# Optimization experiments

Measured on AMD Instinct MI355X. Metric: run time of the kernel, lower is better.

Reference implementation:

```python
import jax, jax.numpy as jnp
import numpy as np

B = 8192
LATENT = 512
HIDDEN = 256
MLP_HIDDEN = 1024
NUM_CLASSES = 2
ODE_STEPS = 100


def setup_inputs() -> dict:
    key = jax.random.key(0)
    ks = jax.random.split(key, 14)
    s = lambda fan_in: 1.0 / np.sqrt(fan_in)
    d = {
        "z": jax.random.normal(ks[0], (B, LATENT), dtype=jnp.float32),
        # real NeuralODE: Linear(latent+1 -> hidden) -> GELU -> Linear(hidden -> latent)
        "real_W1": jax.random.uniform(ks[1], (LATENT + 1, HIDDEN), jnp.float32, -s(LATENT + 1), s(LATENT + 1)),
        "real_b1": jax.random.uniform(ks[2], (HIDDEN,), jnp.float32, -s(LATENT + 1), s(LATENT + 1)),
        "real_W2": jax.random.uniform(ks[3], (HIDDEN, LATENT), jnp.float32, -s(HIDDEN), s(HIDDEN)),
        "real_b2": jax.random.uniform(ks[4], (LATENT,), jnp.float32, -s(HIDDEN), s(HIDDEN)),
        # fake NeuralODE
        "fake_W1": jax.random.uniform(ks[5], (LATENT + 1, HIDDEN), jnp.float32, -s(LATENT + 1), s(LATENT + 1)),
        "fake_b1": jax.random.uniform(ks[6], (HIDDEN,), jnp.float32, -s(LATENT + 1), s(LATENT + 1)),
        "fake_W2": jax.random.uniform(ks[7], (HIDDEN, LATENT), jnp.float32, -s(HIDDEN), s(HIDDEN)),
        "fake_b2": jax.random.uniform(ks[8], (LATENT,), jnp.float32, -s(HIDDEN), s(HIDDEN)),
        # classifier MLP: Linear(2*latent -> mlp_hidden) -> GELU -> Linear(mlp_hidden -> num_classes)
        "mlp_W1": jax.random.uniform(ks[9], (2 * LATENT, MLP_HIDDEN), jnp.float32, -s(2 * LATENT), s(2 * LATENT)),
        "mlp_b1": jax.random.uniform(ks[10], (MLP_HIDDEN,), jnp.float32, -s(2 * LATENT), s(2 * LATENT)),
        "mlp_W2": jax.random.uniform(ks[11], (MLP_HIDDEN, NUM_CLASSES), jnp.float32, -s(MLP_HIDDEN), s(MLP_HIDDEN)),
        "mlp_b2": jax.random.uniform(ks[12], (NUM_CLASSES,), jnp.float32, -s(MLP_HIDDEN), s(MLP_HIDDEN)),
    }
    return d


def _ode_net(z, t, W1, b1, W2, b2):
    # z: [B, latent], t: [B, 1] -> velocity [B, latent]
    inp = jnp.concatenate([z, t], axis=1)
    h = jax.nn.gelu(inp @ W1 + b1, approximate=False)
    return h @ W2 + b2


def _inv_sample(z, W1, b1, W2, b2, N):
    dt = 1.0 / N
    ones = jnp.ones((z.shape[0], 1), dtype=z.dtype)

    def step(z, i):
        t = ones * (i.astype(z.dtype) / N)  # [B, 1]
        pred = _ode_net(z, 1.0 - t, W1, b1, W2, b2)
        return z - pred * dt, None

    z, _ = jax.lax.scan(step, z, jnp.arange(N))
    return z


def reference(z, real_W1, real_b1, real_W2, real_b2,
              fake_W1, fake_b1, fake_W2, fake_b2,
              mlp_W1, mlp_b1, mlp_W2, mlp_b2):
    real_proj = _inv_sample(z, real_W1, real_b1, real_W2, real_b2, ODE_STEPS)
    fake_proj = _inv_sample(z, fake_W1, fake_b1, fake_W2, fake_b2, ODE_STEPS)
    combined = jnp.concatenate([real_proj, fake_proj], axis=1)  # [B, 2*latent]
    h = jax.nn.gelu(combined @ mlp_W1 + mlp_b1, approximate=False)
    logits = h @ mlp_W2 + mlp_b2  # [B, num_classes]
    return logits
```

## Files before the change

kernel.cpp:

```cpp
#include <hip/hip_runtime.h>
#include <hip/hip_bf16.h>

typedef __attribute__((ext_vector_type(8))) short short8;
typedef __attribute__((ext_vector_type(4))) short short4_;
typedef __attribute__((ext_vector_type(4))) float f32x4;
typedef __attribute__((ext_vector_type(2))) unsigned int uint2_;

#define MFMA16(a,b,c) __builtin_amdgcn_mfma_f32_16x16x32_bf16((a),(b),(c),0,0,0)

#define BAR() do {                                         \
  __builtin_amdgcn_sched_barrier(0);                       \
  asm volatile("s_waitcnt lgkmcnt(0)" ::: "memory");       \
  __builtin_amdgcn_s_barrier();                            \
  __builtin_amdgcn_sched_barrier(0);                       \
} while (0)

__device__ __forceinline__ short f2bf(float f){
  union { float f; unsigned u; } v; v.f = f;
  unsigned u = v.u;
  u = u + 0x7fffu + ((u >> 16) & 1u);
  return (short)(u >> 16);
}

__device__ __forceinline__ unsigned cvt_pk_bf16(float lo, float hi){
  unsigned r;
  asm("v_cvt_pk_bf16_f32 %0, %1, %2" : "=v"(r) : "v"(lo), "v"(hi));
  return r;
}

__device__ __forceinline__ float gelu_f(float x){
  float x2 = x * x;
  float t  = __builtin_fmaf(0.044715f, x2, 1.0f);
  float u  = 2.30211416f * x * t;
  float e  = __builtin_exp2f(u);
  float r  = __builtin_amdgcn_rcpf(e + 1.0f);
  return x * (1.0f - r);
}

__global__ void prep_kernel(
    const float* __restrict__ rW1, const float* __restrict__ rW2,
    const float* __restrict__ fW1, const float* __restrict__ fW2,
    const float* __restrict__ mW1,
    short* __restrict__ w1t_all, short* __restrict__ w2t_all,
    short* __restrict__ mw1t)
{
  int id = blockIdx.x * 256 + threadIdx.x;
  short8 v;
  if (id < 32768) {
    int l = id & 63, ks = (id >> 6) & 15, nt = (id >> 10) & 15, net = id >> 14;
    const float* W = net ? fW1 : rW1;
    int n  = nt * 16 + (l & 15);
    int k0 = ks * 32 + (l >> 4) * 8;
    #pragma unroll
    for (int j = 0; j < 8; ++j) v[j] = f2bf(W[(size_t)(k0 + j) * 256 + n]);
    *(short8*)(w1t_all + (size_t)id * 8) = v;
  } else if (id < 65536) {
    int id2 = id - 32768;
    int l = id2 & 63, ks = (id2 >> 6) & 7, nt = (id2 >> 9) & 31, net = id2 >> 14;
    const float* W = net ? fW2 : rW2;
    int n  = nt * 16 + (l & 15);
    int k0 = ks * 32 + (l >> 4) * 8;
    #pragma unroll
    for (int j = 0; j < 8; ++j) v[j] = f2bf(W[(size_t)(k0 + j) * 512 + n]);
    *(short8*)(w2t_all + (size_t)id2 * 8) = v;
  } else {
    int id3 = id - 65536;
    int l = id3 & 63, ks = (id3 >> 6) & 31, nt = id3 >> 11;
    int n  = nt * 16 + (l & 15);
    int k0 = ks * 32 + (l >> 4) * 8;
    #pragma unroll
    for (int j = 0; j < 8; ++j) v[j] = f2bf(mW1[(size_t)(k0 + j) * 1024 + n]);
    *(short8*)(mw1t + (size_t)id3 * 8) = v;
  }
}

#define LDW1(nt, ks) (*(const short8*)(w1t + ((size_t)(((2 * w + (nt)) * 16 + (ks)) * 64 + l) * 8)))
#define LDW2(nt, ks) (*(const short8*)(w2t + ((size_t)(((4 * w + (nt)) * 8  + (ks)) * 64 + l) * 8)))

__global__ __launch_bounds__(512) __attribute__((amdgpu_waves_per_eu(2)))
void ode_kernel(
    const float* __restrict__ z0,
    const short* __restrict__ w1t_all,
    const short* __restrict__ w2t_all,
    const float* __restrict__ rW1, const float* __restrict__ rb1, const float* __restrict__ rb2,
    const float* __restrict__ fW1, const float* __restrict__ fb1, const float* __restrict__ fb2,
    short* __restrict__ proj_all)
{
  __shared__ __align__(16) short zs[32768];
  __shared__ __align__(16) short hs[16384];
  __shared__ __align__(16) float cst[1024];

  const int blk = blockIdx.x;
  const int net = blk & 1;
  const int m0  = (blk >> 1) * 64;
  const int tid = threadIdx.x;
  const int w   = tid >> 6;
  const int l   = tid & 63;
  const int l4  = l & 15;
  const int g   = l >> 4;

  const short* w1t = w1t_all + net * 131072;
  const short* w2t = w2t_all + net * 131072;
  const float* b1p = net ? fb1 : rb1;
  const float* b2p = net ? fb2 : rb2;
  const float* w1r = (net ? fW1 : rW1) + 512 * 256;
  short* proj = proj_all + (size_t)net * (8192 * 512);

  if (tid < 256)       cst[tid] = b1p[tid];
  else                 cst[tid] = w1r[tid - 256];
  cst[512 + tid] = -0.01f * b2p[tid];

  f32x4 zacc[4][4];
  #pragma unroll
  for (int nt = 0; nt < 4; ++nt)
    #pragma unroll
    for (int mt = 0; mt < 4; ++mt)
      zacc[nt][mt] = *(const f32x4*)(z0 + (size_t)(m0 + 16 * mt + l4) * 512
                                        + (64 * w + 16 * nt + 4 * g));

  short8 pA0, pB0, pA1, pB1;
  short8 q00, q01, q02, q03;
  short8 q10, q11, q12, q13;

#define G1F(ks, pa, pb, ...) do {                                              \
    _Pragma("unroll")                                                          \
    for (int mt = 0; mt < 4; ++mt){                                            \
      int m  = 16 * mt + l4;                                                   \
      int kk = (ks) * 32 + 8 * g;                                              \
      short8 b = *(const short8*)((const char*)zs +                            \
                   (m * 1024 + ((kk * 2) ^ ((m & 7) << 4))));                  \
      hacc[0][mt] = MFMA16(pa, b, hacc[0][mt]);                                \
      hacc[1][mt] = MFMA16(pb, b, hacc[1][mt]);                                \
    }                                                                          \
    __VA_ARGS__;                                                               \
  } while (0)

#define G2K(ks, qa, qb, qc, qd, ...) do {                                      \
    _Pragma("unroll")                                                          \
    for (int mt = 0; mt < 4; ++mt){                                            \
      int m  = 16 * mt + l4;                                                   \
      int kk = (ks) * 32 + 8 * g;                                              \
      short8 b = *(const short8*)((const char*)hs +                            \
                   (m * 512 + ((kk * 2) ^ ((m & 7) << 4))));                   \
      zacc[0][mt] = MFMA16(qa, b, zacc[0][mt]);                                \
      zacc[1][mt] = MFMA16(qb, b, zacc[1][mt]);                                \
      zacc[2][mt] = MFMA16(qc, b, zacc[2][mt]);                                \
      zacc[3][mt] = MFMA16(qd, b, zacc[3][mt]);                                \
    }                                                                          \
    __VA_ARGS__;                                                               \
  } while (0)

#define GELU_STORE(NT) do {                                                    \
    f32x4 b1q = *(const f32x4*)&cst[32 * w + 16 * (NT) + 4 * g];               \
    f32x4 w1q = *(const f32x4*)&cst[256 + 32 * w + 16 * (NT) + 4 * g];         \
    _Pragma("unroll")                                                          \
    for (int mt = 0; mt < 4; ++mt){                                            \
      int m = 16 * mt + l4;                                                    \
      float gv[4];                                                             \
      _Pragma("unroll")                                                        \
      for (int r = 0; r < 4; ++r){                                             \
        float x  = hacc[NT][mt][r] + __builtin_fmaf(tw, w1q[r], b1q[r]);       \
        float x2 = x * x;                                                      \
        float tt = __builtin_fmaf(0.044715f, x2, 1.0f);                        \
        float uu = 2.30211416f * x * tt;                                       \
        float ee = __builtin_exp2f(uu);                                        \
        float rr = __builtin_amdgcn_rcpf(ee + 1.0f);                           \
        float xs = -0.01f * x;                                                 \
        gv[r] = __builtin_fmaf(-xs, rr, xs);                    \
      }                                                                        \
      uint2_ pk;                                                               \
      pk[0] = cvt_pk_bf16(gv[0], gv[1]);                                       \
      pk[1] = cvt_pk_bf16(gv[2], gv[3]);                                       \
      int nq = 32 * w + 16 * (NT) + 4 * g;                                     \
      int byte = m * 512 + ((nq * 2) ^ ((m & 7) << 4));                        \
      *(uint2_*)((char*)hs + byte) = pk;                                       \
    }                                                                          \
  } while (0)

  for (int i = 0; i < 100; ++i){
    float tw = 1.0f - 0.01f * (float)i;

    pA0 = LDW1(0, 0); pB0 = LDW1(1, 0);
    pA1 = LDW1(0, 1); pB1 = LDW1(1, 1);

    #pragma unroll
    for (int nt = 0; nt < 4; ++nt)
      #pragma unroll
      for (int mt = 0; mt < 4; ++mt){
        int m  = 16 * mt + l4;
        int kq = 64 * w + 16 * nt + 4 * g;
        uint2_ pk;
        pk[0] = cvt_pk_bf16(zacc[nt][mt][0], zacc[nt][mt][1]);
        pk[1] = cvt_pk_bf16(zacc[nt][mt][2], zacc[nt][mt][3]);
        int byte = m * 1024 + ((kq * 2) ^ ((m & 7) << 4));
        *(uint2_*)((char*)zs + byte) = pk;
      }
    BAR();

    f32x4 hacc[2][4];
    #pragma unroll
    for (int nt = 0; nt < 2; ++nt)
      #pragma unroll
      for (int mt = 0; mt < 4; ++mt) hacc[nt][mt] = (f32x4){0.f,0.f,0.f,0.f};

    G1F( 0, pA0, pB0, pA0 = LDW1(0, 2);  pB0 = LDW1(1, 2));
    G1F( 1, pA1, pB1, pA1 = LDW1(0, 3);  pB1 = LDW1(1, 3));
    G1F( 2, pA0, pB0, pA0 = LDW1(0, 4);  pB0 = LDW1(1, 4));
    G1F( 3, pA1, pB1, pA1 = LDW1(0, 5);  pB1 = LDW1(1, 5));
    G1F( 4, pA0, pB0, pA0 = LDW1(0, 6);  pB0 = LDW1(1, 6));
    G1F( 5, pA1, pB1, pA1 = LDW1(0, 7);  pB1 = LDW1(1, 7));
    G1F( 6, pA0, pB0, pA0 = LDW1(0, 8);  pB0 = LDW1(1, 8));
    G1F( 7, pA1, pB1, pA1 = LDW1(0, 9);  pB1 = LDW1(1, 9));
    G1F( 8, pA0, pB0, pA0 = LDW1(0,10);  pB0 = LDW1(1,10));
    G1F( 9, pA1, pB1, pA1 = LDW1(0,11);  pB1 = LDW1(1,11));
    G1F(10, pA0, pB0, pA0 = LDW1(0,12);  pB0 = LDW1(1,12));
    G1F(11, pA1, pB1, pA1 = LDW1(0,13);  pB1 = LDW1(1,13));
    G1F(12, pA0, pB0, pA0 = LDW1(0,14);  pB0 = LDW1(1,14));
    G1F(13, pA1, pB1, pA1 = LDW1(0,15);  pB1 = LDW1(1,15));
    G1F(14, pA0, pB0, );
    G1F(15, pA1, pB1, );

    q00 = LDW2(0,0); q01 = LDW2(1,0); q02 = LDW2(2,0); q03 = LDW2(3,0);

    GELU_STORE(0);
    GELU_STORE(1);

    q10 = LDW2(0,1); q11 = LDW2(1,1); q12 = LDW2(2,1); q13 = LDW2(3,1);
    BAR();

    G2K(0, q00, q01, q02, q03, q00=LDW2(0,2); q01=LDW2(1,2); q02=LDW2(2,2); q03=LDW2(3,2));
    G2K(1, q10, q11, q12, q13, q10=LDW2(0,3); q11=LDW2(1,3); q12=LDW2(2,3); q13=LDW2(3,3));
    G2K(2, q00, q01, q02, q03, q00=LDW2(0,4); q01=LDW2(1,4); q02=LDW2(2,4); q03=LDW2(3,4));
    G2K(3, q10, q11, q12, q13, q10=LDW2(0,5); q11=LDW2(1,5); q12=LDW2(2,5); q13=LDW2(3,5));
    G2K(4, q00, q01, q02, q03, q00=LDW2(0,6); q01=LDW2(1,6); q02=LDW2(2,6); q03=LDW2(3,6));
    G2K(5, q10, q11, q12, q13, q10=LDW2(0,7); q11=LDW2(1,7); q12=LDW2(2,7); q13=LDW2(3,7));
    G2K(6, q00, q01, q02, q03, );
    G2K(7, q10, q11, q12, q13, );

    #pragma unroll
    for (int nt = 0; nt < 4; ++nt){
      f32x4 b2q = *(const f32x4*)&cst[512 + 64 * w + 16 * nt + 4 * g];
      #pragma unroll
      for (int mt = 0; mt < 4; ++mt)
        #pragma unroll
        for (int r = 0; r < 4; ++r)
          zacc[nt][mt][r] += b2q[r];
    }
  }
#undef G1F
#undef G2K
#undef GELU_STORE

  #pragma unroll
  for (int nt = 0; nt < 4; ++nt)
    #pragma unroll
    for (int mt = 0; mt < 4; ++mt){
      int mg = m0 + 16 * mt + l4;
      int nq = 64 * w + 16 * nt + 4 * g;
      uint2_ pk;
      pk[0] = cvt_pk_bf16(zacc[nt][mt][0], zacc[nt][mt][1]);
      pk[1] = cvt_pk_bf16(zacc[nt][mt][2], zacc[nt][mt][3]);
      *(uint2_*)(proj + (size_t)mg * 512 + nq) = pk;
    }
}

__global__ __launch_bounds__(512, 2) void cls_kernel(
    const short* __restrict__ mw1t,
    const short* __restrict__ proj_all,
    const float* __restrict__ mb1,
    const float* __restrict__ mw2,
    const float* __restrict__ mb2,
    float* __restrict__ out)
{
  __shared__ __align__(16) float sb1[1024];
  __shared__ __align__(16) float sw2[2048];
  __shared__ __align__(16) float sred[2048];

  const int blk = blockIdx.x;
  const int m0  = blk * 32;
  const int tid = threadIdx.x;
  const int w = tid >> 6, l = tid & 63, l4 = l & 15, g = l >> 4;

  #pragma unroll
  for (int j = 0; j < 2; ++j) sb1[tid + 512 * j] = mb1[tid + 512 * j];
  #pragma unroll
  for (int j = 0; j < 4; ++j) sw2[tid + 512 * j] = mw2[tid + 512 * j];
  __syncthreads();

  float lacc[2][2] = {{0.f, 0.f}, {0.f, 0.f}};

  for (int rnd = 0; rnd < 4; ++rnd){
    f32x4 hacc[2][2];
    #pragma unroll
    for (int nt = 0; nt < 2; ++nt)
      #pragma unroll
      for (int mt = 0; mt < 2; ++mt)
        hacc[nt][mt] = (f32x4){0.f, 0.f, 0.f, 0.f};

    #pragma unroll
    for (int ks = 0; ks < 32; ++ks){
      int gnt0 = rnd * 16 + 2 * w;
      short8 a0 = *(const short8*)(mw1t + ((size_t)((gnt0    ) * 32 + ks) * 64 + l) * 8);
      short8 a1 = *(const short8*)(mw1t + ((size_t)((gnt0 + 1) * 32 + ks) * 64 + l) * 8);
      int k = ks * 32 + 8 * g;
      const short* src = (k < 512) ? (proj_all + k)
                                   : (proj_all + ((size_t)8192 * 512 - 512) + k);
      #pragma unroll
      for (int mt = 0; mt < 2; ++mt){
        int mg = m0 + 16 * mt + l4;
        short8 b = *(const short8*)(src + (size_t)mg * 512);
        hacc[0][mt] = MFMA16(a0, b, hacc[0][mt]);
        hacc[1][mt] = MFMA16(a1, b, hacc[1][mt]);
      }
    }
    #pragma unroll
    for (int nt = 0; nt < 2; ++nt){
      int nq = (rnd * 16 + 2 * w + nt) * 16 + 4 * g;
      f32x4 bb = *(const f32x4*)(sb1 + nq);
      #pragma unroll
      for (int r = 0; r < 4; ++r){
        float w2c0 = sw2[(nq + r) * 2 + 0];
        float w2c1 = sw2[(nq + r) * 2 + 1];
        #pragma unroll
        for (int mt = 0; mt < 2; ++mt){
          float x  = hacc[nt][mt][r] + bb[r];
          float gv = gelu_f(x);
          lacc[mt][0] = __builtin_fmaf(gv, w2c0, lacc[mt][0]);
          lacc[mt][1] = __builtin_fmaf(gv, w2c1, lacc[mt][1]);
        }
      }
    }
  }

  int part = w * 4 + g;
  #pragma unroll
  for (int mt = 0; mt < 2; ++mt)
    #pragma unroll
    for (int c = 0; c < 2; ++c)
      sred[((16 * mt + l4) * 2 + c) * 32 + part] = lacc[mt][c];
  __syncthreads();
  if (tid < 64){
    int m = tid >> 1, c = tid & 1;
    float s = 0.f;
    #pragma unroll
    for (int p2 = 0; p2 < 32; ++p2) s += sred[(m * 2 + c) * 32 + p2];
    out[(size_t)(m0 + m) * 2 + c] = s + mb2[c];
  }
}

extern "C" void kernel_launch(void* const* d_in, const int* in_sizes, int n_in,
                              void* d_out, int out_size, void* d_ws, size_t ws_size,
                              hipStream_t stream)
{
  const float* z0  = (const float*)d_in[0];
  const float* rW1 = (const float*)d_in[1];
  const float* rb1 = (const float*)d_in[2];
  const float* rW2 = (const float*)d_in[3];
  const float* rb2 = (const float*)d_in[4];
  const float* fW1 = (const float*)d_in[5];
  const float* fb1 = (const float*)d_in[6];
  const float* fW2 = (const float*)d_in[7];
  const float* fb2 = (const float*)d_in[8];
  const float* mW1 = (const float*)d_in[9];
  const float* mb1 = (const float*)d_in[10];
  const float* mW2 = (const float*)d_in[11];
  const float* mb2 = (const float*)d_in[12];
  float* out = (float*)d_out;

  char* ws = (char*)d_ws;
  short* w1t_all = (short*)(ws);
  short* w2t_all = (short*)(ws + 524288);
  short* mw1t    = (short*)(ws + 1048576);
  short* proj    = (short*)(ws + 3145728);

  prep_kernel<<<768, 256, 0, stream>>>(rW1, rW2, fW1, fW2, mW1, w1t_all, w2t_all, mw1t);
  ode_kernel<<<256, 512, 0, stream>>>(z0, w1t_all, w2t_all,
                                      rW1, rb1, rb2, fW1, fb1, fb2, proj);
  cls_kernel<<<256, 512, 0, stream>>>(mw1t, proj, mb1, mW2, mb2, out);
}
```

Before: 1.039 ms.

## Split ODE block rows across 16 waves instead of 8

Doubles the ODE kernel block to 1024 threads. Each wave now covers half of the 64-row tile (two m-tiles) for the same output columns, which halves per-wave accumulators and MFMA work per step. The goal is more waves per CU to hide LDS and weight-load latency across the 100 sequential steps. In exchange every wave reloads the same weight fragments from global/L2, so weight traffic per block doubles, and barriers now synchronise 16 waves.

```diff
diff --git a/kernel.cpp b/kernel.cpp
--- a/kernel.cpp
+++ b/kernel.cpp
@@ -74,11 +74,10 @@
   }
 }
 
-#define LDW1(nt, ks) (*(const short8*)(w1t + ((size_t)(((2 * w + (nt)) * 16 + (ks)) * 64 + l) * 8)))
-#define LDW2(nt, ks) (*(const short8*)(w2t + ((size_t)(((4 * w + (nt)) * 8  + (ks)) * 64 + l) * 8)))
-
-__global__ __launch_bounds__(512) __attribute__((amdgpu_waves_per_eu(2)))
-void ode_kernel(
+#define LDW1(nt, ks) (*(const short8*)(w1t + ((size_t)(((2 * wh + (nt)) * 16 + (ks)) * 64 + l) * 8)))
+#define LDW2(nt, ks) (*(const short8*)(w2t + ((size_t)(((4 * wh + (nt)) * 8  + (ks)) * 64 + l) * 8)))
+
+__global__ __launch_bounds__(1024) void ode_kernel(
     const float* __restrict__ z0,
     const short* __restrict__ w1t_all,
     const short* __restrict__ w2t_all,
@@ -95,6 +94,8 @@
   const int m0  = (blk >> 1) * 64;
   const int tid = threadIdx.x;
   const int w   = tid >> 6;
+  const int wh  = w & 7;
+  const int mh  = w >> 3;
   const int l   = tid & 63;
   const int l4  = l & 15;
   const int g   = l >> 4;
@@ -107,16 +108,16 @@
   short* proj = proj_all + (size_t)net * (8192 * 512);
 
   if (tid < 256)       cst[tid] = b1p[tid];
-  else                 cst[tid] = w1r[tid - 256];
-  cst[512 + tid] = -0.01f * b2p[tid];
-
-  f32x4 zacc[4][4];
+  else if (tid < 512)  cst[tid] = w1r[tid - 256];
+  else                 cst[tid] = -0.01f * b2p[tid - 512];
+
+  f32x4 zacc[4][2];
   #pragma unroll
   for (int nt = 0; nt < 4; ++nt)
     #pragma unroll
-    for (int mt = 0; mt < 4; ++mt)
-      zacc[nt][mt] = *(const f32x4*)(z0 + (size_t)(m0 + 16 * mt + l4) * 512
-                                        + (64 * w + 16 * nt + 4 * g));
+    for (int mtl = 0; mtl < 2; ++mtl)
+      zacc[nt][mtl] = *(const f32x4*)(z0 + (size_t)(m0 + 16 * (2 * mh + mtl) + l4) * 512
+                                         + (64 * wh + 16 * nt + 4 * g));
 
   short8 pA0, pB0, pA1, pB1;
   short8 q00, q01, q02, q03;
@@ -124,42 +125,42 @@
 
 #define G1F(ks, pa, pb, ...) do {                                              \
     _Pragma("unroll")                                                          \
-    for (int mt = 0; mt < 4; ++mt){                                            \
-      int m  = 16 * mt + l4;                                                   \
+    for (int mtl = 0; mtl < 2; ++mtl){                                         \
+      int m  = 16 * (2 * mh + mtl) + l4;                                       \
       int kk = (ks) * 32 + 8 * g;                                              \
       short8 b = *(const short8*)((const char*)zs +                            \
                    (m * 1024 + ((kk * 2) ^ ((m & 7) << 4))));                  \
-      hacc[0][mt] = MFMA16(pa, b, hacc[0][mt]);                                \
-      hacc[1][mt] = MFMA16(pb, b, hacc[1][mt]);                                \
+      hacc[0][mtl] = MFMA16(pa, b, hacc[0][mtl]);                              \
+      hacc[1][mtl] = MFMA16(pb, b, hacc[1][mtl]);                              \
     }                                                                          \
     __VA_ARGS__;                                                               \
   } while (0)
 
 #define G2K(ks, qa, qb, qc, qd, ...) do {                                      \
     _Pragma("unroll")                                                          \
-    for (int mt = 0; mt < 4; ++mt){                                            \
-      int m  = 16 * mt + l4;                                                   \
+    for (int mtl = 0; mtl < 2; ++mtl){                                         \
+      int m  = 16 * (2 * mh + mtl) + l4;                                       \
       int kk = (ks) * 32 + 8 * g;                                              \
       short8 b = *(const short8*)((const char*)hs +                            \
                    (m * 512 + ((kk * 2) ^ ((m & 7) << 4))));                   \
-      zacc[0][mt] = MFMA16(qa, b, zacc[0][mt]);                                \
-      zacc[1][mt] = MFMA16(qb, b, zacc[1][mt]);                                \
-      zacc[2][mt] = MFMA16(qc, b, zacc[2][mt]);                                \
-      zacc[3][mt] = MFMA16(qd, b, zacc[3][mt]);                                \
+      zacc[0][mtl] = MFMA16(qa, b, zacc[0][mtl]);                              \
+      zacc[1][mtl] = MFMA16(qb, b, zacc[1][mtl]);                              \
+      zacc[2][mtl] = MFMA16(qc, b, zacc[2][mtl]);                              \
+      zacc[3][mtl] = MFMA16(qd, b, zacc[3][mtl]);                              \
     }                                                                          \
     __VA_ARGS__;                                                               \
   } while (0)
 
 #define GELU_STORE(NT) do {                                                    \
-    f32x4 b1q = *(const f32x4*)&cst[32 * w + 16 * (NT) + 4 * g];               \
-    f32x4 w1q = *(const f32x4*)&cst[256 + 32 * w + 16 * (NT) + 4 * g];         \
+    f32x4 b1q = *(const f32x4*)&cst[32 * wh + 16 * (NT) + 4 * g];              \
+    f32x4 w1q = *(const f32x4*)&cst[256 + 32 * wh + 16 * (NT) + 4 * g];        \
     _Pragma("unroll")                                                          \
-    for (int mt = 0; mt < 4; ++mt){                                            \
-      int m = 16 * mt + l4;                                                    \
+    for (int mtl = 0; mtl < 2; ++mtl){                                         \
+      int m = 16 * (2 * mh + mtl) + l4;                                        \
       float gv[4];                                                             \
       _Pragma("unroll")                                                        \
       for (int r = 0; r < 4; ++r){                                             \
-        float x  = hacc[NT][mt][r] + __builtin_fmaf(tw, w1q[r], b1q[r]);       \
+        float x  = hacc[NT][mtl][r] + __builtin_fmaf(tw, w1q[r], b1q[r]);      \
         float x2 = x * x;                                                      \
         float tt = __builtin_fmaf(0.044715f, x2, 1.0f);                        \
         float uu = 2.30211416f * x * tt;                                       \
@@ -171,7 +172,7 @@
       uint2_ pk;                                                               \
       pk[0] = cvt_pk_bf16(gv[0], gv[1]);                                       \
       pk[1] = cvt_pk_bf16(gv[2], gv[3]);                                       \
-      int nq = 32 * w + 16 * (NT) + 4 * g;                                     \
+      int nq = 32 * wh + 16 * (NT) + 4 * g;                                    \
       int byte = m * 512 + ((nq * 2) ^ ((m & 7) << 4));                        \
       *(uint2_*)((char*)hs + byte) = pk;                                       \
     }                                                                          \
@@ -186,22 +187,22 @@
     #pragma unroll
     for (int nt = 0; nt < 4; ++nt)
       #pragma unroll
-      for (int mt = 0; mt < 4; ++mt){
-        int m  = 16 * mt + l4;
-        int kq = 64 * w + 16 * nt + 4 * g;
+      for (int mtl = 0; mtl < 2; ++mtl){
+        int m  = 16 * (2 * mh + mtl) + l4;
+        int kq = 64 * wh + 16 * nt + 4 * g;
         uint2_ pk;
-        pk[0] = cvt_pk_bf16(zacc[nt][mt][0], zacc[nt][mt][1]);
-        pk[1] = cvt_pk_bf16(zacc[nt][mt][2], zacc[nt][mt][3]);
+        pk[0] = cvt_pk_bf16(zacc[nt][mtl][0], zacc[nt][mtl][1]);
+        pk[1] = cvt_pk_bf16(zacc[nt][mtl][2], zacc[nt][mtl][3]);
         int byte = m * 1024 + ((kq * 2) ^ ((m & 7) << 4));
         *(uint2_*)((char*)zs + byte) = pk;
       }
     BAR();
 
-    f32x4 hacc[2][4];
+    f32x4 hacc[2][2];
     #pragma unroll
     for (int nt = 0; nt < 2; ++nt)
       #pragma unroll
-      for (int mt = 0; mt < 4; ++mt) hacc[nt][mt] = (f32x4){0.f,0.f,0.f,0.f};
+      for (int mtl = 0; mtl < 2; ++mtl) hacc[nt][mtl] = (f32x4){0.f,0.f,0.f,0.f};
 
     G1F( 0, pA0, pB0, pA0 = LDW1(0, 2);  pB0 = LDW1(1, 2));
     G1F( 1, pA1, pB1, pA1 = LDW1(0, 3);  pB1 = LDW1(1, 3));
@@ -239,12 +240,12 @@
 
     #pragma unroll
     for (int nt = 0; nt < 4; ++nt){
-      f32x4 b2q = *(const f32x4*)&cst[512 + 64 * w + 16 * nt + 4 * g];
-      #pragma unroll
-      for (int mt = 0; mt < 4; ++mt)
+      f32x4 b2q = *(const f32x4*)&cst[512 + 64 * wh + 16 * nt + 4 * g];
+      #pragma unroll
+      for (int mtl = 0; mtl < 2; ++mtl)
         #pragma unroll
         for (int r = 0; r < 4; ++r)
-          zacc[nt][mt][r] += b2q[r];
+          zacc[nt][mtl][r] += b2q[r];
     }
   }
 #undef G1F
@@ -254,12 +255,12 @@
   #pragma unroll
   for (int nt = 0; nt < 4; ++nt)
     #pragma unroll
-    for (int mt = 0; mt < 4; ++mt){
-      int mg = m0 + 16 * mt + l4;
-      int nq = 64 * w + 16 * nt + 4 * g;
+    for (int mtl = 0; mtl < 2; ++mtl){
+      int mg = m0 + 16 * (2 * mh + mtl) + l4;
+      int nq = 64 * wh + 16 * nt + 4 * g;
       uint2_ pk;
-      pk[0] = cvt_pk_bf16(zacc[nt][mt][0], zacc[nt][mt][1]);
-      pk[1] = cvt_pk_bf16(zacc[nt][mt][2], zacc[nt][mt][3]);
+      pk[0] = cvt_pk_bf16(zacc[nt][mtl][0], zacc[nt][mtl][1]);
+      pk[1] = cvt_pk_bf16(zacc[nt][mtl][2], zacc[nt][mtl][3]);
       *(uint2_*)(proj + (size_t)mg * 512 + nq) = pk;
     }
 }
@@ -374,7 +375,7 @@
   short* proj    = (short*)(ws + 3145728);
 
   prep_kernel<<<768, 256, 0, stream>>>(rW1, rW2, fW1, fW2, mW1, w1t_all, w2t_all, mw1t);
-  ode_kernel<<<256, 512, 0, stream>>>(z0, w1t_all, w2t_all,
-                                      rW1, rb1, rb2, fW1, fb1, fb2, proj);
+  ode_kernel<<<256, 1024, 0, stream>>>(z0, w1t_all, w2t_all,
+                                       rW1, rb1, rb2, fW1, fb1, fb2, proj);
   cls_kernel<<<256, 512, 0, stream>>>(mw1t, proj, mb1, mW2, mb2, out);
 }
```

New measurement: 2.551 ms. 2.46x slower.

## Split ODE blocks to 32 rows with 4 waves each for more blocks

Applied to the files above, without the earlier changes.

Retiles the ODE kernel so each block handles 32 batch rows with 256 threads (4 waves) instead of 64 rows with 8 waves, launching 512 blocks instead of 256. Each wave now covers twice as many output columns (64 hidden, 128 latent) and holds 4/8 weight fragments per k-step. The aim is to fill more CUs on a 256-CU device and cut barrier cost, since fewer waves sync per step. In exchange, each weight fragment fetched is reused over half as many rows, which doubles total weight traffic per step, and register pressure per wave rises.

```diff
diff --git a/kernel.cpp b/kernel.cpp
--- a/kernel.cpp
+++ b/kernel.cpp
@@ -74,10 +74,10 @@
   }
 }
 
-#define LDW1(nt, ks) (*(const short8*)(w1t + ((size_t)(((2 * w + (nt)) * 16 + (ks)) * 64 + l) * 8)))
-#define LDW2(nt, ks) (*(const short8*)(w2t + ((size_t)(((4 * w + (nt)) * 8  + (ks)) * 64 + l) * 8)))
-
-__global__ __launch_bounds__(512) __attribute__((amdgpu_waves_per_eu(2)))
+#define LDW1(nt, ks) (*(const short8*)(w1t + ((size_t)(((4 * wv + (nt)) * 16 + (ks)) * 64 + l) * 8)))
+#define LDW2(nt, ks) (*(const short8*)(w2t + ((size_t)(((8 * wv + (nt)) * 8  + (ks)) * 64 + l) * 8)))
+
+__global__ __launch_bounds__(256) __attribute__((amdgpu_waves_per_eu(2)))
 void ode_kernel(
     const float* __restrict__ z0,
     const short* __restrict__ w1t_all,
@@ -86,15 +86,15 @@
     const float* __restrict__ fW1, const float* __restrict__ fb1, const float* __restrict__ fb2,
     short* __restrict__ proj_all)
 {
-  __shared__ __align__(16) short zs[32768];
-  __shared__ __align__(16) short hs[16384];
+  __shared__ __align__(16) short zs[16384];
+  __shared__ __align__(16) short hs[8192];
   __shared__ __align__(16) float cst[1024];
 
   const int blk = blockIdx.x;
   const int net = blk & 1;
-  const int m0  = (blk >> 1) * 64;
+  const int m0  = (blk >> 1) * 32;
   const int tid = threadIdx.x;
-  const int w   = tid >> 6;
+  const int wv  = tid >> 6;
   const int l   = tid & 63;
   const int l4  = l & 15;
   const int g   = l >> 4;
@@ -106,55 +106,63 @@
   const float* w1r = (net ? fW1 : rW1) + 512 * 256;
   short* proj = proj_all + (size_t)net * (8192 * 512);
 
-  if (tid < 256)       cst[tid] = b1p[tid];
-  else                 cst[tid] = w1r[tid - 256];
+  cst[tid]       = b1p[tid];
+  cst[256 + tid] = w1r[tid];
   cst[512 + tid] = -0.01f * b2p[tid];
-
-  f32x4 zacc[4][4];
+  cst[768 + tid] = -0.01f * b2p[256 + tid];
+
+  f32x4 zacc[8][2];
   #pragma unroll
-  for (int nt = 0; nt < 4; ++nt)
-    #pragma unroll
-    for (int mt = 0; mt < 4; ++mt)
+  for (int nt = 0; nt < 8; ++nt)
+    #pragma unroll
+    for (int mt = 0; mt < 2; ++mt)
       zacc[nt][mt] = *(const f32x4*)(z0 + (size_t)(m0 + 16 * mt + l4) * 512
-                                        + (64 * w + 16 * nt + 4 * g));
-
-  short8 pA0, pB0, pA1, pB1;
-  short8 q00, q01, q02, q03;
-  short8 q10, q11, q12, q13;
-
-#define G1F(ks, pa, pb, ...) do {                                              \
+                                        + (128 * wv + 16 * nt + 4 * g));
+
+  short8 pA0, pA1, pA2, pA3;
+  short8 pB0, pB1, pB2, pB3;
+  short8 qa0, qa1, qa2, qa3, qa4, qa5, qa6, qa7;
+  short8 qb0, qb1, qb2, qb3, qb4, qb5, qb6, qb7;
+
+#define G1F(ks, f0, f1, f2, f3, ...) do {                                      \
     _Pragma("unroll")                                                          \
-    for (int mt = 0; mt < 4; ++mt){                                            \
+    for (int mt = 0; mt < 2; ++mt){                                            \
       int m  = 16 * mt + l4;                                                   \
       int kk = (ks) * 32 + 8 * g;                                              \
       short8 b = *(const short8*)((const char*)zs +                            \
                    (m * 1024 + ((kk * 2) ^ ((m & 7) << 4))));                  \
-      hacc[0][mt] = MFMA16(pa, b, hacc[0][mt]);                                \
-      hacc[1][mt] = MFMA16(pb, b, hacc[1][mt]);                                \
+      hacc[0][mt] = MFMA16(f0, b, hacc[0][mt]);                                \
+      hacc[1][mt] = MFMA16(f1, b, hacc[1][mt]);                                \
+      hacc[2][mt] = MFMA16(f2, b, hacc[2][mt]);                                \
+      hacc[3][mt] = MFMA16(f3, b, hacc[3][mt]);                                \
     }                                                                          \
     __VA_ARGS__;                                                               \
   } while (0)
 
-#define G2K(ks, qa, qb, qc, qd, ...) do {                                      \
+#define G2K(ks, f0, f1, f2, f3, f4, f5, f6, f7, ...) do {                      \
     _Pragma("unroll")                                                          \
-    for (int mt = 0; mt < 4; ++mt){                                            \
+    for (int mt = 0; mt < 2; ++mt){                                            \
       int m  = 16 * mt + l4;                                                   \
       int kk = (ks) * 32 + 8 * g;                                              \
       short8 b = *(const short8*)((const char*)hs +                            \
                    (m * 512 + ((kk * 2) ^ ((m & 7) << 4))));                   \
-      zacc[0][mt] = MFMA16(qa, b, zacc[0][mt]);                                \
-      zacc[1][mt] = MFMA16(qb, b, zacc[1][mt]);                                \
-      zacc[2][mt] = MFMA16(qc, b, zacc[2][mt]);                                \
-      zacc[3][mt] = MFMA16(qd, b, zacc[3][mt]);                                \
+      zacc[0][mt] = MFMA16(f0, b, zacc[0][mt]);                                \
+      zacc[1][mt] = MFMA16(f1, b, zacc[1][mt]);                                \
+      zacc[2][mt] = MFMA16(f2, b, zacc[2][mt]);                                \
+      zacc[3][mt] = MFMA16(f3, b, zacc[3][mt]);                                \
+      zacc[4][mt] = MFMA16(f4, b, zacc[4][mt]);                                \
+      zacc[5][mt] = MFMA16(f5, b, zacc[5][mt]);                                \
+      zacc[6][mt] = MFMA16(f6, b, zacc[6][mt]);                                \
+      zacc[7][mt] = MFMA16(f7, b, zacc[7][mt]);                                \
     }                                                                          \
     __VA_ARGS__;                                                               \
   } while (0)
 
 #define GELU_STORE(NT) do {                                                    \
-    f32x4 b1q = *(const f32x4*)&cst[32 * w + 16 * (NT) + 4 * g];               \
-    f32x4 w1q = *(const f32x4*)&cst[256 + 32 * w + 16 * (NT) + 4 * g];         \
+    f32x4 b1q = *(const f32x4*)&cst[64 * wv + 16 * (NT) + 4 * g];              \
+    f32x4 w1q = *(const f32x4*)&cst[256 + 64 * wv + 16 * (NT) + 4 * g];        \
     _Pragma("unroll")                                                          \
-    for (int mt = 0; mt < 4; ++mt){                                            \
+    for (int mt = 0; mt < 2; ++mt){                                            \
       int m = 16 * mt + l4;                                                    \
       float gv[4];                                                             \
       _Pragma("unroll")                                                        \
@@ -171,7 +179,7 @@
       uint2_ pk;                                                               \
       pk[0] = cvt_pk_bf16(gv[0], gv[1]);                                       \
       pk[1] = cvt_pk_bf16(gv[2], gv[3]);                                       \
-      int nq = 32 * w + 16 * (NT) + 4 * g;                                     \
+      int nq = 64 * wv + 16 * (NT) + 4 * g;                                    \
       int byte = m * 512 + ((nq * 2) ^ ((m & 7) << 4));                        \
       *(uint2_*)((char*)hs + byte) = pk;                                       \
     }                                                                          \
@@ -180,15 +188,15 @@
   for (int i = 0; i < 100; ++i){
     float tw = 1.0f - 0.01f * (float)i;
 
-    pA0 = LDW1(0, 0); pB0 = LDW1(1, 0);
-    pA1 = LDW1(0, 1); pB1 = LDW1(1, 1);
-
-    #pragma unroll
-    for (int nt = 0; nt < 4; ++nt)
-      #pragma unroll
-      for (int mt = 0; mt < 4; ++mt){
+    pA0 = LDW1(0, 0); pA1 = LDW1(1, 0); pA2 = LDW1(2, 0); pA3 = LDW1(3, 0);
+    pB0 = LDW1(0, 1); pB1 = LDW1(1, 1); pB2 = LDW1(2, 1); pB3 = LDW1(3, 1);
+
+    #pragma unroll
+    for (int nt = 0; nt < 8; ++nt)
+      #pragma unroll
+      for (int mt = 0; mt < 2; ++mt){
         int m  = 16 * mt + l4;
-        int kq = 64 * w + 16 * nt + 4 * g;
+        int kq = 128 * wv + 16 * nt + 4 * g;
         uint2_ pk;
         pk[0] = cvt_pk_bf16(zacc[nt][mt][0], zacc[nt][mt][1]);
         pk[1] = cvt_pk_bf16(zacc[nt][mt][2], zacc[nt][mt][3]);
@@ -197,51 +205,67 @@
       }
     BAR();
 
-    f32x4 hacc[2][4];
-    #pragma unroll
-    for (int nt = 0; nt < 2; ++nt)
-      #pragma unroll
-      for (int mt = 0; mt < 4; ++mt) hacc[nt][mt] = (f32x4){0.f,0.f,0.f,0.f};
-
-    G1F( 0, pA0, pB0, pA0 = LDW1(0, 2);  pB0 = LDW1(1, 2));
-    G1F( 1, pA1, pB1, pA1 = LDW1(0, 3);  pB1 = LDW1(1, 3));
-    G1F( 2, pA0, pB0, pA0 = LDW1(0, 4);  pB0 = LDW1(1, 4));
-    G1F( 3, pA1, pB1, pA1 = LDW1(0, 5);  pB1 = LDW1(1, 5));
-    G1F( 4, pA0, pB0, pA0 = LDW1(0, 6);  pB0 = LDW1(1, 6));
-    G1F( 5, pA1, pB1, pA1 = LDW1(0, 7);  pB1 = LDW1(1, 7));
-    G1F( 6, pA0, pB0, pA0 = LDW1(0, 8);  pB0 = LDW1(1, 8));
-    G1F( 7, pA1, pB1, pA1 = LDW1(0, 9);  pB1 = LDW1(1, 9));
-    G1F( 8, pA0, pB0, pA0 = LDW1(0,10);  pB0 = LDW1(1,10));
-    G1F( 9, pA1, pB1, pA1 = LDW1(0,11);  pB1 = LDW1(1,11));
-    G1F(10, pA0, pB0, pA0 = LDW1(0,12);  pB0 = LDW1(1,12));
-    G1F(11, pA1, pB1, pA1 = LDW1(0,13);  pB1 = LDW1(1,13));
-    G1F(12, pA0, pB0, pA0 = LDW1(0,14);  pB0 = LDW1(1,14));
-    G1F(13, pA1, pB1, pA1 = LDW1(0,15);  pB1 = LDW1(1,15));
-    G1F(14, pA0, pB0, );
-    G1F(15, pA1, pB1, );
-
-    q00 = LDW2(0,0); q01 = LDW2(1,0); q02 = LDW2(2,0); q03 = LDW2(3,0);
+    f32x4 hacc[4][2];
+    #pragma unroll
+    for (int nt = 0; nt < 4; ++nt)
+      #pragma unroll
+      for (int mt = 0; mt < 2; ++mt) hacc[nt][mt] = (f32x4){0.f,0.f,0.f,0.f};
+
+    G1F( 0, pA0,pA1,pA2,pA3, pA0=LDW1(0, 2); pA1=LDW1(1, 2); pA2=LDW1(2, 2); pA3=LDW1(3, 2));
+    G1F( 1, pB0,pB1,pB2,pB3, pB0=LDW1(0, 3); pB1=LDW1(1, 3); pB2=LDW1(2, 3); pB3=LDW1(3, 3));
+    G1F( 2, pA0,pA1,pA2,pA3, pA0=LDW1(0, 4); pA1=LDW1(1, 4); pA2=LDW1(2, 4); pA3=LDW1(3, 4));
+    G1F( 3, pB0,pB1,pB2,pB3, pB0=LDW1(0, 5); pB1=LDW1(1, 5); pB2=LDW1(2, 5); pB3=LDW1(3, 5));
+    G1F( 4, pA0,pA1,pA2,pA3, pA0=LDW1(0, 6); pA1=LDW1(1, 6); pA2=LDW1(2, 6); pA3=LDW1(3, 6));
+    G1F( 5, pB0,pB1,pB2,pB3, pB0=LDW1(0, 7); pB1=LDW1(1, 7); pB2=LDW1(2, 7); pB3=LDW1(3, 7));
+    G1F( 6, pA0,pA1,pA2,pA3, pA0=LDW1(0, 8); pA1=LDW1(1, 8); pA2=LDW1(2, 8); pA3=LDW1(3, 8));
+    G1F( 7, pB0,pB1,pB2,pB3, pB0=LDW1(0, 9); pB1=LDW1(1, 9); pB2=LDW1(2, 9); pB3=LDW1(3, 9));
+    G1F( 8, pA0,pA1,pA2,pA3, pA0=LDW1(0,10); pA1=LDW1(1,10); pA2=LDW1(2,10); pA3=LDW1(3,10));
+    G1F( 9, pB0,pB1,pB2,pB3, pB0=LDW1(0,11); pB1=LDW1(1,11); pB2=LDW1(2,11); pB3=LDW1(3,11));
+    G1F(10, pA0,pA1,pA2,pA3, pA0=LDW1(0,12); pA1=LDW1(1,12); pA2=LDW1(2,12); pA3=LDW1(3,12));
+    G1F(11, pB0,pB1,pB2,pB3, pB0=LDW1(0,13); pB1=LDW1(1,13); pB2=LDW1(2,13); pB3=LDW1(3,13));
+    G1F(12, pA0,pA1,pA2,pA3, pA0=LDW1(0,14); pA1=LDW1(1,14); pA2=LDW1(2,14); pA3=LDW1(3,14));
+    G1F(13, pB0,pB1,pB2,pB3, pB0=LDW1(0,15); pB1=LDW1(1,15); pB2=LDW1(2,15); pB3=LDW1(3,15));
+    G1F(14, pA0,pA1,pA2,pA3,
+        qa0=LDW2(0,0); qa1=LDW2(1,0); qa2=LDW2(2,0); qa3=LDW2(3,0);
+        qa4=LDW2(4,0); qa5=LDW2(5,0); qa6=LDW2(6,0); qa7=LDW2(7,0));
+    G1F(15, pB0,pB1,pB2,pB3, );
 
     GELU_STORE(0);
     GELU_STORE(1);
 
-    q10 = LDW2(0,1); q11 = LDW2(1,1); q12 = LDW2(2,1); q13 = LDW2(3,1);
+    qb0=LDW2(0,1); qb1=LDW2(1,1); qb2=LDW2(2,1); qb3=LDW2(3,1);
+    qb4=LDW2(4,1); qb5=LDW2(5,1); qb6=LDW2(6,1); qb7=LDW2(7,1);
+
+    GELU_STORE(2);
+    GELU_STORE(3);
     BAR();
 
-    G2K(0, q00, q01, q02, q03, q00=LDW2(0,2); q01=LDW2(1,2); q02=LDW2(2,2); q03=LDW2(3,2));
-    G2K(1, q10, q11, q12, q13, q10=LDW2(0,3); q11=LDW2(1,3); q12=LDW2(2,3); q13=LDW2(3,3));
-    G2K(2, q00, q01, q02, q03, q00=LDW2(0,4); q01=LDW2(1,4); q02=LDW2(2,4); q03=LDW2(3,4));
-    G2K(3, q10, q11, q12, q13, q10=LDW2(0,5); q11=LDW2(1,5); q12=LDW2(2,5); q13=LDW2(3,5));
-    G2K(4, q00, q01, q02, q03, q00=LDW2(0,6); q01=LDW2(1,6); q02=LDW2(2,6); q03=LDW2(3,6));
-    G2K(5, q10, q11, q12, q13, q10=LDW2(0,7); q11=LDW2(1,7); q12=LDW2(2,7); q13=LDW2(3,7));
-    G2K(6, q00, q01, q02, q03, );
-    G2K(7, q10, q11, q12, q13, );
-
-    #pragma unroll
-    for (int nt = 0; nt < 4; ++nt){
-      f32x4 b2q = *(const f32x4*)&cst[512 + 64 * w + 16 * nt + 4 * g];
-      #pragma unroll
-      for (int mt = 0; mt < 4; ++mt)
+    G2K(0, qa0,qa1,qa2,qa3,qa4,qa5,qa6,qa7,
+        qa0=LDW2(0,2); qa1=LDW2(1,2); qa2=LDW2(2,2); qa3=LDW2(3,2);
+        qa4=LDW2(4,2); qa5=LDW2(5,2); qa6=LDW2(6,2); qa7=LDW2(7,2));
+    G2K(1, qb0,qb1,qb2,qb3,qb4,qb5,qb6,qb7,
+        qb0=LDW2(0,3); qb1=LDW2(1,3); qb2=LDW2(2,3); qb3=LDW2(3,3);
+        qb4=LDW2(4,3); qb5=LDW2(5,3); qb6=LDW2(6,3); qb7=LDW2(7,3));
+    G2K(2, qa0,qa1,qa2,qa3,qa4,qa5,qa6,qa7,
+        qa0=LDW2(0,4); qa1=LDW2(1,4); qa2=LDW2(2,4); qa3=LDW2(3,4);
+        qa4=LDW2(4,4); qa5=LDW2(5,4); qa6=LDW2(6,4); qa7=LDW2(7,4));
+    G2K(3, qb0,qb1,qb2,qb3,qb4,qb5,qb6,qb7,
+        qb0=LDW2(0,5); qb1=LDW2(1,5); qb2=LDW2(2,5); qb3=LDW2(3,5);
+        qb4=LDW2(4,5); qb5=LDW2(5,5); qb6=LDW2(6,5); qb7=LDW2(7,5));
+    G2K(4, qa0,qa1,qa2,qa3,qa4,qa5,qa6,qa7,
+        qa0=LDW2(0,6); qa1=LDW2(1,6); qa2=LDW2(2,6); qa3=LDW2(3,6);
+        qa4=LDW2(4,6); qa5=LDW2(5,6); qa6=LDW2(6,6); qa7=LDW2(7,6));
+    G2K(5, qb0,qb1,qb2,qb3,qb4,qb5,qb6,qb7,
+        qb0=LDW2(0,7); qb1=LDW2(1,7); qb2=LDW2(2,7); qb3=LDW2(3,7);
+        qb4=LDW2(4,7); qb5=LDW2(5,7); qb6=LDW2(6,7); qb7=LDW2(7,7));
+    G2K(6, qa0,qa1,qa2,qa3,qa4,qa5,qa6,qa7, );
+    G2K(7, qb0,qb1,qb2,qb3,qb4,qb5,qb6,qb7, );
+
+    #pragma unroll
+    for (int nt = 0; nt < 8; ++nt){
+      f32x4 b2q = *(const f32x4*)&cst[512 + 128 * wv + 16 * nt + 4 * g];
+      #pragma unroll
+      for (int mt = 0; mt < 2; ++mt)
         #pragma unroll
         for (int r = 0; r < 4; ++r)
           zacc[nt][mt][r] += b2q[r];
@@ -252,11 +276,11 @@
 #undef GELU_STORE
 
   #pragma unroll
-  for (int nt = 0; nt < 4; ++nt)
-    #pragma unroll
-    for (int mt = 0; mt < 4; ++mt){
+  for (int nt = 0; nt < 8; ++nt)
+    #pragma unroll
+    for (int mt = 0; mt < 2; ++mt){
       int mg = m0 + 16 * mt + l4;
-      int nq = 64 * w + 16 * nt + 4 * g;
+      int nq = 128 * wv + 16 * nt + 4 * g;
       uint2_ pk;
       pk[0] = cvt_pk_bf16(zacc[nt][mt][0], zacc[nt][mt][1]);
       pk[1] = cvt_pk_bf16(zacc[nt][mt][2], zacc[nt][mt][3]);
@@ -374,7 +398,7 @@
   short* proj    = (short*)(ws + 3145728);
 
   prep_kernel<<<768, 256, 0, stream>>>(rW1, rW2, fW1, fW2, mW1, w1t_all, w2t_all, mw1t);
-  ode_kernel<<<256, 512, 0, stream>>>(z0, w1t_all, w2t_all,
+  ode_kernel<<<512, 256, 0, stream>>>(z0, w1t_all, w2t_all,
                                       rW1, rb1, rb2, fW1, fb1, fb2, proj);
   cls_kernel<<<256, 512, 0, stream>>>(mw1t, proj, mb1, mW2, mb2, out);
 }
```

Measured after the change: 3.265 ms. +214.3%, slower.
